# Performance work log

Measured on AMD Instinct MI355X. Metric: run time of the kernel, lower is better.

The kernel has to match this reference:

```python
import jax, jax.numpy as jnp
import numpy as np

C = 256
NUM_HEADS = 8
NUM_GROUPS = 32
EPS = 1e-5


def setup_inputs() -> dict:
    key = jax.random.key(0)
    ks = jax.random.split(key, 7)
    B, H, W = 2, 64, 64
    x = jax.random.normal(ks[0], (B, C, H, W), dtype=jnp.float32)
    norm_gamma = jnp.ones((C,), dtype=jnp.float32)
    norm_beta = jnp.zeros((C,), dtype=jnp.float32)
    # 1x1 convs == per-pixel linear layers; store weights as (out_ch, in_ch)
    qkv_w = jax.random.normal(ks[1], (3 * C, C), dtype=jnp.float32) * (1.0 / np.sqrt(C))
    qkv_b = jnp.zeros((3 * C,), dtype=jnp.float32)
    proj_w = jax.random.normal(ks[2], (C, C), dtype=jnp.float32) * (1.0 / np.sqrt(C))
    proj_b = jnp.zeros((C,), dtype=jnp.float32)
    return {"x": x, "norm_gamma": norm_gamma, "norm_beta": norm_beta,
            "qkv_w": qkv_w, "qkv_b": qkv_b, "proj_w": proj_w, "proj_b": proj_b}


def _group_norm(x, gamma, beta):
    B, Cc, H, W = x.shape
    xg = x.reshape(B, NUM_GROUPS, Cc // NUM_GROUPS, H, W)
    mean = xg.mean(axis=(2, 3, 4), keepdims=True)
    var = xg.var(axis=(2, 3, 4), keepdims=True)
    xn = ((xg - mean) * jax.lax.rsqrt(var + EPS)).reshape(B, Cc, H, W)
    return xn * gamma[None, :, None, None] + beta[None, :, None, None]


def reference(x, norm_gamma, norm_beta, qkv_w, qkv_b, proj_w, proj_b):
    B, Cc, H, W = x.shape
    hd = Cc // NUM_HEADS
    N = H * W

    h = _group_norm(x, norm_gamma, norm_beta)
    # 1x1 conv: (3C,C) x (B,C,H,W) -> (B,3C,H,W)
    qkv = jnp.einsum('oc,bchw->bohw', qkv_w, h) + qkv_b[None, :, None, None]
    q, k, v = jnp.split(qkv, 3, axis=1)

    def heads(t):  # (B,C,H,W) -> (B,heads,N,hd)
        return t.reshape(B, NUM_HEADS, hd, N).transpose(0, 1, 3, 2)

    q, k, v = heads(q), heads(k), heads(v)
    scale = hd ** (-0.5)
    attn = jax.nn.softmax(jnp.einsum('bhnd,bhmd->bhnm', q, k) * scale, axis=-1)
    out = jnp.einsum('bhnm,bhmd->bhnd', attn, v)  # (B,heads,N,hd)
    out = out.transpose(0, 1, 3, 2).reshape(B, Cc, H, W)
    out = jnp.einsum('oc,bchw->bohw', proj_w, out) + proj_b[None, :, None, None]
    return x + out
```

## Files before the change

kernel.cpp:

```cpp
#include <hip/hip_runtime.h>
#include <math.h>

#define C_    256
#define NH    8
#define HD_   32
#define NG    32
#define CPG   8
#define NPIX  4096
#define BATCH 2
#define EPSV  1e-5f
#define SLOG2 0.25503489f
#define MF    16.0f
#define KVB   64
#define KSTR  40
#define VSTR  72
#define KPS2  2048

typedef __bf16 bf16x8 __attribute__((ext_vector_type(8)));
typedef __bf16 bf16x4 __attribute__((ext_vector_type(4)));
typedef float  f32x4  __attribute__((ext_vector_type(4)));

__global__ __launch_bounds__(256) void prep_kernel(const float* __restrict__ x,
                                                   float* __restrict__ stats,
                                                   const float* __restrict__ qw,
                                                   const float* __restrict__ pw,
                                                   __bf16* __restrict__ wbq,
                                                   __bf16* __restrict__ wbp) {
    if (blockIdx.x >= 64) {
        const int i = ((blockIdx.x - 64) * 256 + threadIdx.x) * 4;
        const float* src;
        __bf16* dst;
        int off;
        if (i < 768 * 256) { src = qw; dst = wbq; off = i; }
        else { src = pw; dst = wbp; off = i - 768 * 256; }
        const float4 v = *(const float4*)(src + off);
        bf16x4 o;
        o[0] = (__bf16)v.x; o[1] = (__bf16)v.y; o[2] = (__bf16)v.z; o[3] = (__bf16)v.w;
        *(bf16x4*)(dst + off) = o;
        return;
    }
    const int blk = blockIdx.x;
    const int b = blk >> 5, g = blk & 31;
    const float* __restrict__ xp = x + ((size_t)(b * C_ + g * CPG)) * NPIX;

    float s = 0.f, ss = 0.f;
    for (int i = threadIdx.x * 4; i < CPG * NPIX; i += 256 * 4) {
        const float4 v = *(const float4*)(xp + i);
        s  += v.x + v.y + v.z + v.w;
        ss += v.x * v.x + v.y * v.y + v.z * v.z + v.w * v.w;
    }
    #pragma unroll
    for (int off = 32; off; off >>= 1) {
        s  += __shfl_down(s, off);
        ss += __shfl_down(ss, off);
    }
    __shared__ float ls[4], lss[4];
    const int wid = threadIdx.x >> 6, lane = threadIdx.x & 63;
    if (lane == 0) { ls[wid] = s; lss[wid] = ss; }
    __syncthreads();
    if (threadIdx.x == 0) {
        float S = 0.f, SS = 0.f;
        #pragma unroll
        for (int w = 0; w < 4; ++w) { S += ls[w]; SS += lss[w]; }
        const float inv_n = 1.0f / (float)(CPG * NPIX);
        const float mean = S * inv_n;
        const float var  = SS * inv_n - mean * mean;
        stats[blk * 2 + 0] = mean;
        stats[blk * 2 + 1] = rsqrtf(var + EPSV);
    }
}

__global__ __launch_bounds__(256) void ht_kernel(const float* __restrict__ x,
                                                 const float* __restrict__ stats,
                                                 const float* __restrict__ gamma,
                                                 const float* __restrict__ beta,
                                                 __bf16* __restrict__ Ht) {
    const int b = blockIdx.y;
    const int n0 = blockIdx.x * 64;
    __shared__ __align__(16) __bf16 tile[64][264];
    const int nn = (threadIdx.x & 15) * 4;
    #pragma unroll
    for (int p = 0; p < 16; ++p) {
        const int c = (threadIdx.x >> 4) + p * 16;
        const float4 v = *(const float4*)(x + ((size_t)(b * C_ + c)) * NPIX + n0 + nn);
        const int g = c >> 3;
        const float mean = stats[(b * NG + g) * 2 + 0];
        const float rstd = stats[(b * NG + g) * 2 + 1];
        const float ga = gamma[c] * rstd;
        const float be = beta[c] - mean * ga;
        tile[nn + 0][c] = (__bf16)(v.x * ga + be);
        tile[nn + 1][c] = (__bf16)(v.y * ga + be);
        tile[nn + 2][c] = (__bf16)(v.z * ga + be);
        tile[nn + 3][c] = (__bf16)(v.w * ga + be);
    }
    __syncthreads();
    #pragma unroll
    for (int p = 0; p < 8; ++p) {
        const int id = p * 256 + threadIdx.x;
        const int row = id >> 5;
        const int ch  = id & 31;
        *(bf16x8*)(Ht + ((size_t)(b * NPIX) + n0 + row) * C_ + ch * 8) =
            *(const bf16x8*)(&tile[row][ch * 8]);
    }
}

__global__ __launch_bounds__(256) void qkv_gemm_kernel(const __bf16* __restrict__ wbq,
                                                       const float* __restrict__ bias,
                                                       const __bf16* __restrict__ Ht,
                                                       __bf16* __restrict__ Qb,
                                                       __bf16* __restrict__ Kb,
                                                       __bf16* __restrict__ Vb) {
    const int b = blockIdx.z;
    const int n0 = blockIdx.x * 32;
    const int wave = threadIdx.x >> 6, lane = threadIdx.x & 63;
    const int col = lane & 15, g = lane >> 4;
    const int m0 = blockIdx.y * 256 + wave * 64;
    const __bf16* __restrict__ hp = Ht + (size_t)b * NPIX * C_;

    f32x4 acc[4][2];
    #pragma unroll
    for (int i = 0; i < 4; ++i)
        #pragma unroll
        for (int j = 0; j < 2; ++j) acc[i][j] = (f32x4){0.f, 0.f, 0.f, 0.f};

    #pragma unroll
    for (int c0 = 0; c0 < C_; c0 += 32) {
        bf16x8 la[4], lb[2];
        #pragma unroll
        for (int mb = 0; mb < 4; ++mb)
            la[mb] = *(const bf16x8*)(wbq + (size_t)(m0 + mb * 16 + col) * C_ + c0 + g * 8);
        #pragma unroll
        for (int nb = 0; nb < 2; ++nb)
            lb[nb] = *(const bf16x8*)(hp + (size_t)(n0 + nb * 16 + col) * C_ + c0 + g * 8);
        #pragma unroll
        for (int mb = 0; mb < 4; ++mb)
            #pragma unroll
            for (int nb = 0; nb < 2; ++nb)
                acc[mb][nb] = __builtin_amdgcn_mfma_f32_16x16x32_bf16(la[mb], lb[nb], acc[mb][nb], 0, 0, 0);
    }

    #pragma unroll
    for (int mb = 0; mb < 4; ++mb) {
        const int mbase = m0 + mb * 16 + 4 * g;
        const float4 b4 = *(const float4*)(bias + mbase);
        const int route = mbase >> 8;
        const int bh = b * NH + ((mbase >> 5) & 7);
        const int d0 = mbase & 31;
        #pragma unroll
        for (int nb = 0; nb < 2; ++nb) {
            const int n = n0 + nb * 16 + col;
            f32x4 v = acc[mb][nb];
            v[0] += b4.x; v[1] += b4.y; v[2] += b4.z; v[3] += b4.w;
            if (route == 0) {
                bf16x4 o;
                #pragma unroll
                for (int r = 0; r < 4; ++r) o[r] = (__bf16)(v[r] * SLOG2);
                *(bf16x4*)(Qb + (((size_t)bh * NPIX + n) << 5) + d0) = o;
            } else if (route == 1) {
                bf16x4 o;
                #pragma unroll
                for (int r = 0; r < 4; ++r) o[r] = (__bf16)v[r];
                *(bf16x4*)(Kb + (((size_t)bh * NPIX + n) << 5) + d0) = o;
            } else {
                #pragma unroll
                for (int r = 0; r < 4; ++r)
                    Vb[((size_t)bh * HD_ + d0 + r) * NPIX + n] = (__bf16)v[r];
            }
        }
    }
}

__global__ __launch_bounds__(512) void attn_kernel(const __bf16* __restrict__ Qb,
                                                   const __bf16* __restrict__ Kb,
                                                   const __bf16* __restrict__ Vb,
                                                   __bf16* __restrict__ aot) {
    __shared__ __align__(16) char smem[38912];
    __bf16 (*Ks)[2][KVB][KSTR] = (__bf16 (*)[2][KVB][KSTR])(smem);
    __bf16 (*Vs)[2][HD_][VSTR] = (__bf16 (*)[2][HD_][VSTR])(smem + 20480);
    float* pbuf = (float*)smem;

    const int b = blockIdx.z, h = blockIdx.y;
    const int wave = threadIdx.x >> 6, lane = threadIdx.x & 63;
    const int hw = wave >> 2, wv = wave & 3;
    const int col = lane & 15, g = lane >> 4;
    const int bh = b * NH + h;
    const int q0 = blockIdx.x * 128 + wv * 32;

    const __bf16* __restrict__ qp = Qb + ((size_t)bh * NPIX + q0) * HD_;
    const __bf16* __restrict__ kp = Kb + ((size_t)bh * NPIX + hw * KPS2) * HD_;
    const __bf16* __restrict__ vp = Vb + (size_t)bh * HD_ * NPIX + hw * KPS2;

    const int sk_key = wv * 16 + (lane >> 2);
    const int sk_seg = (lane & 3) * 8;
    const int sv_d   = wv * 8 + (lane >> 3);
    const int sv_seg = (lane & 7) * 8;
    const int vslot  = (sv_seg & 32) + ((((sv_seg & 15) >> 2) << 3)) + (((sv_seg >> 4) & 1) << 2);
    const __bf16* __restrict__ kg = kp + (size_t)sk_key * HD_ + sk_seg;
    const __bf16* __restrict__ vg = vp + (size_t)sv_d * NPIX + sv_seg;

    const bf16x8 fq0 = *(const bf16x8*)(qp + col * HD_ + g * 8);
    const bf16x8 fq1 = *(const bf16x8*)(qp + (16 + col) * HD_ + g * 8);

    bf16x8 ones;
    #pragma unroll
    for (int j = 0; j < 8; ++j) ones[j] = (__bf16)1.0f;
    const f32x4 mfc = {-MF, -MF, -MF, -MF};

    f32x4 acc00 = {0.f,0.f,0.f,0.f}, acc01 = {0.f,0.f,0.f,0.f};
    f32x4 acc10 = {0.f,0.f,0.f,0.f}, acc11 = {0.f,0.f,0.f,0.f};
    f32x4 accL0 = {0.f,0.f,0.f,0.f}, accL1 = {0.f,0.f,0.f,0.f};

    {
        const bf16x8 rk = *(const bf16x8*)(kg);
        const bf16x8 rv = *(const bf16x8*)(vg);
        *(bf16x8*)&Ks[hw][0][sk_key][sk_seg] = rk;
        bf16x4 lo, hi;
        #pragma unroll
        for (int j = 0; j < 4; ++j) { lo[j] = rv[j]; hi[j] = rv[4 + j]; }
        *(bf16x4*)&Vs[hw][0][sv_d][vslot]     = lo;
        *(bf16x4*)&Vs[hw][0][sv_d][vslot + 8] = hi;
    }
    __syncthreads();

    const int nt = KPS2 / KVB;
    for (int t = 0; t < nt; ++t) {
        const int cur = t & 1;
        bf16x8 nk, nv;
        const bool more = (t + 1 < nt);
        {
            const size_t koff = (size_t)(more ? (t + 1) * KVB : 0);
            nk = *(const bf16x8*)(kg + koff * HD_);
            nv = *(const bf16x8*)(vg + koff);
        }

        #pragma unroll
        for (int kk = 0; kk < KVB; kk += 32) {
            const bf16x8 fk0 = *(const bf16x8*)(&Ks[hw][cur][kk + col][g * 8]);
            const bf16x8 fk1 = *(const bf16x8*)(&Ks[hw][cur][kk + 16 + col][g * 8]);
            const bf16x8 fv0 = *(const bf16x8*)(&Vs[hw][cur][col][kk + 8 * g]);
            const bf16x8 fv1 = *(const bf16x8*)(&Vs[hw][cur][col + 16][kk + 8 * g]);

            __builtin_amdgcn_s_setprio(1);
            f32x4 s00 = __builtin_amdgcn_mfma_f32_16x16x32_bf16(fk0, fq0, mfc, 0, 0, 0);
            f32x4 s10 = __builtin_amdgcn_mfma_f32_16x16x32_bf16(fk1, fq0, mfc, 0, 0, 0);
            f32x4 s01 = __builtin_amdgcn_mfma_f32_16x16x32_bf16(fk0, fq1, mfc, 0, 0, 0);
            f32x4 s11 = __builtin_amdgcn_mfma_f32_16x16x32_bf16(fk1, fq1, mfc, 0, 0, 0);
            __builtin_amdgcn_s_setprio(0);

            float p0[8], p1[8];
            #pragma unroll
            for (int r = 0; r < 4; ++r) {
                p0[r]     = __builtin_amdgcn_exp2f(s00[r]);
                p0[4 + r] = __builtin_amdgcn_exp2f(s10[r]);
                p1[r]     = __builtin_amdgcn_exp2f(s01[r]);
                p1[4 + r] = __builtin_amdgcn_exp2f(s11[r]);
            }

            bf16x8 fp0, fp1;
            #pragma unroll
            for (int j = 0; j < 8; ++j) { fp0[j] = (__bf16)p0[j]; fp1[j] = (__bf16)p1[j]; }

            __builtin_amdgcn_s_setprio(1);
            accL0 = __builtin_amdgcn_mfma_f32_16x16x32_bf16(ones, fp0, accL0, 0, 0, 0);
            accL1 = __builtin_amdgcn_mfma_f32_16x16x32_bf16(ones, fp1, accL1, 0, 0, 0);
            acc00 = __builtin_amdgcn_mfma_f32_16x16x32_bf16(fv0, fp0, acc00, 0, 0, 0);
            acc01 = __builtin_amdgcn_mfma_f32_16x16x32_bf16(fv1, fp0, acc01, 0, 0, 0);
            acc10 = __builtin_amdgcn_mfma_f32_16x16x32_bf16(fv0, fp1, acc10, 0, 0, 0);
            acc11 = __builtin_amdgcn_mfma_f32_16x16x32_bf16(fv1, fp1, acc11, 0, 0, 0);
            __builtin_amdgcn_s_setprio(0);
        }

        if (more) {
            *(bf16x8*)&Ks[hw][cur ^ 1][sk_key][sk_seg] = nk;
            bf16x4 lo, hi;
            #pragma unroll
            for (int j = 0; j < 4; ++j) { lo[j] = nv[j]; hi[j] = nv[4 + j]; }
            *(bf16x4*)&Vs[hw][cur ^ 1][sv_d][vslot]     = lo;
            *(bf16x4*)&Vs[hw][cur ^ 1][sv_d][vslot + 8] = hi;
        }
        __syncthreads();
    }

    float l0 = accL0[0], l1 = accL1[0];

    if (hw == 1) {
        float* pp = pbuf + ((size_t)wv * 64 + lane) * 20;
        *(f32x4*)(pp + 0)  = acc00;
        *(f32x4*)(pp + 4)  = acc01;
        *(f32x4*)(pp + 8)  = acc10;
        *(f32x4*)(pp + 12) = acc11;
        pp[16] = l0; pp[17] = l1;
    }
    __syncthreads();
    if (hw == 0) {
        const float* pp = pbuf + ((size_t)wv * 64 + lane) * 20;
        const f32x4 b00 = *(const f32x4*)(pp + 0);
        const f32x4 b01 = *(const f32x4*)(pp + 4);
        const f32x4 b10 = *(const f32x4*)(pp + 8);
        const f32x4 b11 = *(const f32x4*)(pp + 12);
        #pragma unroll
        for (int r = 0; r < 4; ++r) {
            acc00[r] += b00[r]; acc01[r] += b01[r];
            acc10[r] += b10[r]; acc11[r] += b11[r];
        }
        const float inv0 = 1.0f / (l0 + pp[16]);
        const float inv1 = 1.0f / (l1 + pp[17]);
        const int cb = h * HD_ + 4 * g;
        {
            __bf16* op = aot + ((size_t)(b * NPIX) + q0 + col) * C_ + cb;
            bf16x4 o0, o1;
            #pragma unroll
            for (int r = 0; r < 4; ++r) { o0[r] = (__bf16)(acc00[r] * inv0); o1[r] = (__bf16)(acc01[r] * inv0); }
            *(bf16x4*)(op) = o0;
            *(bf16x4*)(op + 16) = o1;
        }
        {
            __bf16* op = aot + ((size_t)(b * NPIX) + q0 + 16 + col) * C_ + cb;
            bf16x4 o0, o1;
            #pragma unroll
            for (int r = 0; r < 4; ++r) { o0[r] = (__bf16)(acc10[r] * inv1); o1[r] = (__bf16)(acc11[r] * inv1); }
            *(bf16x4*)(op) = o0;
            *(bf16x4*)(op + 16) = o1;
        }
    }
}

__global__ __launch_bounds__(256) void proj_gemm_kernel(const __bf16* __restrict__ wbp,
                                                        const float* __restrict__ bias,
                                                        const __bf16* __restrict__ aot,
                                                        const float* __restrict__ x,
                                                        float* __restrict__ out) {
    const int b = blockIdx.z;
    const int wave = threadIdx.x >> 6, lane = threadIdx.x & 63;
    const int col = lane & 15, g = lane >> 4;
    const int n0 = blockIdx.x * 64 + (wave & 1) * 32;
    const int m0 = blockIdx.y * 64 + (wave >> 1) * 32;
    const __bf16* __restrict__ ap = aot + (size_t)b * NPIX * C_;

    f32x4 acc[2][2];
    #pragma unroll
    for (int i = 0; i < 2; ++i)
        #pragma unroll
        for (int j = 0; j < 2; ++j) acc[i][j] = (f32x4){0.f, 0.f, 0.f, 0.f};

    #pragma unroll
    for (int c0 = 0; c0 < C_; c0 += 32) {
        bf16x8 la[2], lb[2];
        #pragma unroll
        for (int mb = 0; mb < 2; ++mb)
            la[mb] = *(const bf16x8*)(wbp + (size_t)(m0 + mb * 16 + col) * C_ + c0 + g * 8);
        #pragma unroll
        for (int nb = 0; nb < 2; ++nb)
            lb[nb] = *(const bf16x8*)(ap + (size_t)(n0 + nb * 16 + col) * C_ + c0 + g * 8);
        #pragma unroll
        for (int mb = 0; mb < 2; ++mb)
            #pragma unroll
            for (int nb = 0; nb < 2; ++nb)
                acc[mb][nb] = __builtin_amdgcn_mfma_f32_16x16x32_bf16(la[mb], lb[nb], acc[mb][nb], 0, 0, 0);
    }

    #pragma unroll
    for (int mb = 0; mb < 2; ++mb) {
        const int mbase = m0 + mb * 16 + 4 * g;
        const float4 b4 = *(const float4*)(bias + mbase);
        const float bias_r[4] = {b4.x, b4.y, b4.z, b4.w};
        #pragma unroll
        for (int nb = 0; nb < 2; ++nb) {
            const int n = n0 + nb * 16 + col;
            #pragma unroll
            for (int r = 0; r < 4; ++r) {
                const size_t idx = ((size_t)(b * C_ + mbase + r)) * NPIX + n;
                out[idx] = acc[mb][nb][r] + bias_r[r] + x[idx];
            }
        }
    }
}

extern "C" void kernel_launch(void* const* d_in, const int* in_sizes, int n_in,
                              void* d_out, int out_size, void* d_ws, size_t ws_size,
                              hipStream_t stream) {
    (void)in_sizes; (void)n_in; (void)out_size; (void)ws_size;
    const float* x      = (const float*)d_in[0];
    const float* gamma  = (const float*)d_in[1];
    const float* beta   = (const float*)d_in[2];
    const float* qkv_w  = (const float*)d_in[3];
    const float* qkv_b  = (const float*)d_in[4];
    const float* proj_w = (const float*)d_in[5];
    const float* proj_b = (const float*)d_in[6];
    float* out = (float*)d_out;

    char* ws = (char*)d_ws;
    __bf16* wbq  = (__bf16*)(ws);
    __bf16* wbp  = (__bf16*)(ws + 0x60000);
    float*  stats= (float*) (ws + 0x80000);
    __bf16* Ht   = (__bf16*)(ws + 0x100000);
    __bf16* Qb   = (__bf16*)(ws + 0x500000);
    __bf16* Kb   = (__bf16*)(ws + 0x900000);
    __bf16* Vb   = (__bf16*)(ws + 0xD00000);
    __bf16* aot  = (__bf16*)(ws + 0x1100000);

    prep_kernel<<<dim3(320), dim3(256), 0, stream>>>(x, stats, qkv_w, proj_w, wbq, wbp);
    ht_kernel<<<dim3(NPIX / 64, BATCH), dim3(256), 0, stream>>>(x, stats, gamma, beta, Ht);
    qkv_gemm_kernel<<<dim3(NPIX / 32, 3, BATCH), dim3(256), 0, stream>>>(wbq, qkv_b, Ht, Qb, Kb, Vb);
    attn_kernel<<<dim3(NPIX / 128, NH, BATCH), dim3(512), 0, stream>>>(Qb, Kb, Vb, aot);
    proj_gemm_kernel<<<dim3(NPIX / 64, C_ / 64, BATCH), dim3(256), 0, stream>>>(wbp, proj_b, aot, x, out);
}
```

Baseline: 93.89 us.

## Fuse GroupNorm transpose into QKV GEMM, remap attention grid, drop setprio

Removes the separate ht_kernel. Each QKV GEMM block now normalizes its 32-pixel slice of x into a shared-memory bf16 tile and reads the B operand from LDS, so the Ht intermediate is no longer written to or read from global memory and one launch disappears. The trade-off is that x normalization is repeated across the 3 blockIdx.y slices, so x is read three times. Separately, the attention grid becomes 1D with the head index in the low bits, which changes block scheduling order and possibly K/V cache locality, and the s_setprio hints around the MFMAs are removed.

```diff
diff --git a/kernel.cpp b/kernel.cpp
--- a/kernel.cpp
+++ b/kernel.cpp
@@ -70,52 +70,42 @@
     }
 }
 
-__global__ __launch_bounds__(256) void ht_kernel(const float* __restrict__ x,
-                                                 const float* __restrict__ stats,
-                                                 const float* __restrict__ gamma,
-                                                 const float* __restrict__ beta,
-                                                 __bf16* __restrict__ Ht) {
-    const int b = blockIdx.y;
-    const int n0 = blockIdx.x * 64;
-    __shared__ __align__(16) __bf16 tile[64][264];
-    const int nn = (threadIdx.x & 15) * 4;
-    #pragma unroll
-    for (int p = 0; p < 16; ++p) {
-        const int c = (threadIdx.x >> 4) + p * 16;
-        const float4 v = *(const float4*)(x + ((size_t)(b * C_ + c)) * NPIX + n0 + nn);
-        const int g = c >> 3;
-        const float mean = stats[(b * NG + g) * 2 + 0];
-        const float rstd = stats[(b * NG + g) * 2 + 1];
-        const float ga = gamma[c] * rstd;
-        const float be = beta[c] - mean * ga;
-        tile[nn + 0][c] = (__bf16)(v.x * ga + be);
-        tile[nn + 1][c] = (__bf16)(v.y * ga + be);
-        tile[nn + 2][c] = (__bf16)(v.z * ga + be);
-        tile[nn + 3][c] = (__bf16)(v.w * ga + be);
-    }
-    __syncthreads();
-    #pragma unroll
-    for (int p = 0; p < 8; ++p) {
-        const int id = p * 256 + threadIdx.x;
-        const int row = id >> 5;
-        const int ch  = id & 31;
-        *(bf16x8*)(Ht + ((size_t)(b * NPIX) + n0 + row) * C_ + ch * 8) =
-            *(const bf16x8*)(&tile[row][ch * 8]);
-    }
-}
-
 __global__ __launch_bounds__(256) void qkv_gemm_kernel(const __bf16* __restrict__ wbq,
                                                        const float* __restrict__ bias,
-                                                       const __bf16* __restrict__ Ht,
+                                                       const float* __restrict__ x,
+                                                       const float* __restrict__ stats,
+                                                       const float* __restrict__ gamma,
+                                                       const float* __restrict__ beta,
                                                        __bf16* __restrict__ Qb,
                                                        __bf16* __restrict__ Kb,
                                                        __bf16* __restrict__ Vb) {
     const int b = blockIdx.z;
     const int n0 = blockIdx.x * 32;
+    __shared__ __align__(16) __bf16 tile[32][264];
+
+    {
+        const int nn = (threadIdx.x & 7) * 4;
+        const int cb = threadIdx.x >> 3;
+        #pragma unroll
+        for (int p = 0; p < 8; ++p) {
+            const int c = cb + p * 32;
+            const float4 v = *(const float4*)(x + ((size_t)(b * C_ + c)) * NPIX + n0 + nn);
+            const int g = c >> 3;
+            const float mean = stats[(b * NG + g) * 2 + 0];
+            const float rstd = stats[(b * NG + g) * 2 + 1];
+            const float ga = gamma[c] * rstd;
+            const float be = beta[c] - mean * ga;
+            tile[nn + 0][c] = (__bf16)(v.x * ga + be);
+            tile[nn + 1][c] = (__bf16)(v.y * ga + be);
+            tile[nn + 2][c] = (__bf16)(v.z * ga + be);
+            tile[nn + 3][c] = (__bf16)(v.w * ga + be);
+        }
+    }
+    __syncthreads();
+
     const int wave = threadIdx.x >> 6, lane = threadIdx.x & 63;
     const int col = lane & 15, g = lane >> 4;
     const int m0 = blockIdx.y * 256 + wave * 64;
-    const __bf16* __restrict__ hp = Ht + (size_t)b * NPIX * C_;
 
     f32x4 acc[4][2];
     #pragma unroll
@@ -131,7 +121,7 @@
             la[mb] = *(const bf16x8*)(wbq + (size_t)(m0 + mb * 16 + col) * C_ + c0 + g * 8);
         #pragma unroll
         for (int nb = 0; nb < 2; ++nb)
-            lb[nb] = *(const bf16x8*)(hp + (size_t)(n0 + nb * 16 + col) * C_ + c0 + g * 8);
+            lb[nb] = *(const bf16x8*)(&tile[nb * 16 + col][c0 + g * 8]);
         #pragma unroll
         for (int mb = 0; mb < 4; ++mb)
             #pragma unroll
@@ -179,12 +169,17 @@
     __bf16 (*Vs)[2][HD_][VSTR] = (__bf16 (*)[2][HD_][VSTR])(smem + 20480);
     float* pbuf = (float*)smem;
 
-    const int b = blockIdx.z, h = blockIdx.y;
+    const int id = blockIdx.x;
+    const int h = id & 7;
+    const int rest = id >> 3;
+    const int b = rest >> 5;
+    const int qt = rest & 31;
+
     const int wave = threadIdx.x >> 6, lane = threadIdx.x & 63;
     const int hw = wave >> 2, wv = wave & 3;
     const int col = lane & 15, g = lane >> 4;
     const int bh = b * NH + h;
-    const int q0 = blockIdx.x * 128 + wv * 32;
+    const int q0 = qt * 128 + wv * 32;
 
     const __bf16* __restrict__ qp = Qb + ((size_t)bh * NPIX + q0) * HD_;
     const __bf16* __restrict__ kp = Kb + ((size_t)bh * NPIX + hw * KPS2) * HD_;
@@ -240,12 +235,10 @@
             const bf16x8 fv0 = *(const bf16x8*)(&Vs[hw][cur][col][kk + 8 * g]);
             const bf16x8 fv1 = *(const bf16x8*)(&Vs[hw][cur][col + 16][kk + 8 * g]);
 
-            __builtin_amdgcn_s_setprio(1);
             f32x4 s00 = __builtin_amdgcn_mfma_f32_16x16x32_bf16(fk0, fq0, mfc, 0, 0, 0);
             f32x4 s10 = __builtin_amdgcn_mfma_f32_16x16x32_bf16(fk1, fq0, mfc, 0, 0, 0);
             f32x4 s01 = __builtin_amdgcn_mfma_f32_16x16x32_bf16(fk0, fq1, mfc, 0, 0, 0);
             f32x4 s11 = __builtin_amdgcn_mfma_f32_16x16x32_bf16(fk1, fq1, mfc, 0, 0, 0);
-            __builtin_amdgcn_s_setprio(0);
 
             float p0[8], p1[8];
             #pragma unroll
@@ -260,14 +253,12 @@
             #pragma unroll
             for (int j = 0; j < 8; ++j) { fp0[j] = (__bf16)p0[j]; fp1[j] = (__bf16)p1[j]; }
 
-            __builtin_amdgcn_s_setprio(1);
             accL0 = __builtin_amdgcn_mfma_f32_16x16x32_bf16(ones, fp0, accL0, 0, 0, 0);
             accL1 = __builtin_amdgcn_mfma_f32_16x16x32_bf16(ones, fp1, accL1, 0, 0, 0);
             acc00 = __builtin_amdgcn_mfma_f32_16x16x32_bf16(fv0, fp0, acc00, 0, 0, 0);
             acc01 = __builtin_amdgcn_mfma_f32_16x16x32_bf16(fv1, fp0, acc01, 0, 0, 0);
             acc10 = __builtin_amdgcn_mfma_f32_16x16x32_bf16(fv0, fp1, acc10, 0, 0, 0);
             acc11 = __builtin_amdgcn_mfma_f32_16x16x32_bf16(fv1, fp1, acc11, 0, 0, 0);
-            __builtin_amdgcn_s_setprio(0);
         }
 
         if (more) {
@@ -393,15 +384,14 @@
     __bf16* wbq  = (__bf16*)(ws);
     __bf16* wbp  = (__bf16*)(ws + 0x60000);
     float*  stats= (float*) (ws + 0x80000);
-    __bf16* Ht   = (__bf16*)(ws + 0x100000);
     __bf16* Qb   = (__bf16*)(ws + 0x500000);
     __bf16* Kb   = (__bf16*)(ws + 0x900000);
     __bf16* Vb   = (__bf16*)(ws + 0xD00000);
     __bf16* aot  = (__bf16*)(ws + 0x1100000);
 
     prep_kernel<<<dim3(320), dim3(256), 0, stream>>>(x, stats, qkv_w, proj_w, wbq, wbp);
-    ht_kernel<<<dim3(NPIX / 64, BATCH), dim3(256), 0, stream>>>(x, stats, gamma, beta, Ht);
-    qkv_gemm_kernel<<<dim3(NPIX / 32, 3, BATCH), dim3(256), 0, stream>>>(wbq, qkv_b, Ht, Qb, Kb, Vb);
-    attn_kernel<<<dim3(NPIX / 128, NH, BATCH), dim3(512), 0, stream>>>(Qb, Kb, Vb, aot);
+    qkv_gemm_kernel<<<dim3(NPIX / 32, 3, BATCH), dim3(256), 0, stream>>>(
+        wbq, qkv_b, x, stats, gamma, beta, Qb, Kb, Vb);
+    attn_kernel<<<dim3(32 * NH * BATCH), dim3(512), 0, stream>>>(Qb, Kb, Vb, aot);
     proj_gemm_kernel<<<dim3(NPIX / 64, C_ / 64, BATCH), dim3(256), 0, stream>>>(wbp, proj_b, aot, x, out);
 }
```

Measured after the change: 88.78 us. 1.06x faster.
